# Performance work log

Hardware: AMD Instinct MI355X
Metric: run time of the kernel (lower is better)

## Reference

```python
import jax, jax.numpy as jnp
import numpy as np
from itertools import permutations

NUM_LAYERS = 3
K = 5  # fixed node degree -> every Hungarian sub-problem is 5x5
# one-hot permutation tensor: P1H[p, r, c] = 1 iff permutation p assigns row r -> col c
PERMS = np.array(list(permutations(range(K))), dtype=np.int32)          # [120, K]
P1H = (PERMS[:, :, None] == np.arange(K)[None, None, :]).astype(np.float32)  # [120, K, K]


def _mlp(x, W1, b1, W2, b2):
    # 2-layer MLP with ReLU (repo's MLP(in, hid, out, 2))
    return jax.nn.relu(x @ W1 + b1) @ W2 + b2


def _sinkhorn(src, itera):
    s = jax.nn.softmax(src, axis=1)  # row-max subtraction is built in
    for i in range(itera):
        s = s / jnp.sum(s, axis=i % 2, keepdims=True)
    return jnp.nan_to_num(s)


def _masked_softmax(src):
    s1 = jnp.nan_to_num(jax.nn.softmax(src, axis=1))
    s2 = jnp.nan_to_num(jax.nn.softmax(src, axis=0))
    return (s1 + s2) * 0.5


def setup_inputs() -> dict:
    key = jax.random.key(0)
    ks = jax.random.split(key, 12)
    n1 = n2 = 1024
    hid = 64
    adj1 = jax.random.randint(ks[0], (n1, K), 0, n1)
    adj2 = jax.random.randint(ks[1], (n2, K), 0, n2)
    # adjacency matrices consistent with the neighbor lists
    G1 = jnp.zeros((n1, n1), jnp.float32).at[jnp.arange(n1)[:, None], adj1].set(1.0)
    G2 = jnp.zeros((n2, n2), jnp.float32).at[jnp.arange(n2)[:, None], adj2].set(1.0)
    s = 0.1
    return {
        'G1': G1, 'G2': G2, 'adj1': adj1, 'adj2': adj2,
        'ro_W1': jax.random.normal(ks[2], (NUM_LAYERS, 1, hid), jnp.float32) * s,
        'ro_b1': jax.random.normal(ks[3], (NUM_LAYERS, hid), jnp.float32) * s,
        'ro_W2': jax.random.normal(ks[4], (NUM_LAYERS, hid, 1), jnp.float32) * s,
        'ro_b2': jax.random.normal(ks[5], (NUM_LAYERS, 1), jnp.float32) * s,
        'fin_W1': jax.random.normal(ks[6], (1, hid), jnp.float32) * s,
        'fin_b1': jax.random.normal(ks[7], (hid,), jnp.float32) * s,
        'fin_W2': jax.random.normal(ks[8], (hid, 1), jnp.float32) * s,
        'fin_b2': jax.random.normal(ks[9], (1,), jnp.float32) * s,
    }


def reference(G1, G2, adj1, adj2, ro_W1, ro_b1, ro_W2, ro_b2, fin_W1, fin_b1, fin_W2, fin_b2):
    n1 = G1.shape[0]
    n2 = G2.shape[0]
    d1 = jnp.sum(G1, axis=1)
    d2 = jnp.sum(G2, axis=1)
    ttheta = jnp.mean(d1)
    # S[i, j, 0] = -|d1[i] - d2[j]|
    S = -jnp.abs(d1[:, None] - d2[None, :])[..., None]  # [n1, n2, 1]
    p1h = jnp.asarray(P1H)
    for li in range(NUM_LAYERS):
        Wn = _sinkhorn(_mlp(S / ttheta, ro_W1[li], ro_b1[li], ro_W2[li], ro_b2[li]).squeeze(-1), 5)
        W = jnp.log(Wn * (n1 * 1.5))
        W = jnp.where(jnp.isneginf(W), jnp.float32(-1e12), W)
        W = jnp.where(jnp.isposinf(W), jnp.float32(1e12), W)
        Wd = jax.lax.stop_gradient(W)  # matches W.detach().numpy()
        # small[a, b, r, c] = Wd[adj1[a, r], adj2[b, c]]  -> [n1, n2, K, K]
        small = jnp.transpose(Wd[adj1][:, :, adj2], (0, 2, 1, 3))
        # exact linear_sum_assignment(-small): maximize sum over the K! permutations
        scores = jnp.einsum('abrc,prc->abp', small, p1h)  # [n1, n2, 120]
        X1 = jnp.max(scores, axis=-1)                      # [n1, n2]
        S = X1[..., None]
    out = _masked_softmax(_mlp(S, fin_W1, fin_b1, fin_W2, fin_b2).squeeze(-1))
    return out
```

## Files before the change

### kernel.cpp

```cpp
#include <hip/hip_runtime.h>
#include <math.h>

#define N 1024
#define NB 256
#define KD 5
#define SL 8
#define NT 126
#define MAGIC 0x13572468
#define FSTRIDE 32
#define FREGION (NB * FSTRIDE + FSTRIDE)


__device__ __forceinline__ float load_sc(const float* p){
  return __hip_atomic_load(p, __ATOMIC_RELAXED, __HIP_MEMORY_SCOPE_AGENT);
}
__device__ __forceinline__ void store_sc(float* p, float v){
  __hip_atomic_store(p, v, __ATOMIC_RELAXED, __HIP_MEMORY_SCOPE_AGENT);
}
__device__ __forceinline__ int load_sci(const int* p){
  return __hip_atomic_load(p, __ATOMIC_RELAXED, __HIP_MEMORY_SCOPE_AGENT);
}
__device__ __forceinline__ void store_sci(int* p, int v){
  __hip_atomic_store(p, v, __ATOMIC_RELAXED, __HIP_MEMORY_SCOPE_AGENT);
}

__device__ __forceinline__ void gbarS(int* flg){
  __builtin_amdgcn_s_waitcnt(0);
  __syncthreads();
  const int t = threadIdx.x, B = blockIdx.x;
  int* go = flg + NB * FSTRIDE;
  if (B == 0){
    if (t > 0 && t < NB){
      while (load_sci(&flg[t * FSTRIDE]) != MAGIC) __builtin_amdgcn_s_sleep(2);
    }
    __syncthreads();
    if (t == 0) store_sci(go, MAGIC);
  } else {
    if (t == 0){
      store_sci(&flg[B * FSTRIDE], MAGIC);
      while (load_sci(go) != MAGIC) __builtin_amdgcn_s_sleep(2);
    }
    __syncthreads();
  }
}

__device__ __forceinline__ float wred_sum(float v){
#pragma unroll
  for (int off = 32; off > 0; off >>= 1) v += __shfl_down(v, off);
  return v;
}
__device__ __forceinline__ void bsum4(float v[4], float* s64){
  float w0 = wred_sum(v[0]), w1 = wred_sum(v[1]), w2 = wred_sum(v[2]), w3 = wred_sum(v[3]);
  __syncthreads();
  int wv = threadIdx.x >> 6;
  if ((threadIdx.x & 63) == 0){ s64[wv*4] = w0; s64[wv*4+1] = w1; s64[wv*4+2] = w2; s64[wv*4+3] = w3; }
  __syncthreads();
  float r0 = 0.f, r1 = 0.f, r2 = 0.f, r3 = 0.f;
#pragma unroll
  for (int i = 0; i < 16; ++i){ r0 += s64[i*4]; r1 += s64[i*4+1]; r2 += s64[i*4+2]; r3 += s64[i*4+3]; }
  v[0] = r0; v[1] = r1; v[2] = r2; v[3] = r3;
}

__device__ __forceinline__ int distinct5(const int* v){
  int c = 0;
#pragma unroll
  for (int r = 0; r < KD; ++r){
    bool dup = false;
#pragma unroll
    for (int s = 0; s < r; ++s) dup = dup || (v[s] == v[r]);
    c += dup ? 0 : 1;
  }
  return c;
}
__device__ __forceinline__ void sort5(int* s){
#pragma unroll
  for (int i = 0; i < 4; ++i)
#pragma unroll
    for (int j = 0; j < 4 - i; ++j){
      int a = s[j], b = s[j+1];
      s[j] = min(a, b); s[j+1] = max(a, b);
    }
}
__device__ __forceinline__ int msrank(const int* c5){
  const int C_[6][5] = { {0,0,0,0,0},
                         {1,1,1,1,1},
                         {1,2,3,4,5},
                         {1,3,6,10,15},
                         {1,4,10,20,35},
                         {1,5,15,35,70} };
  int rank = 0, prev = 0;
#pragma unroll
  for (int i = 0; i < 5; ++i){
    for (int v = prev; v < c5[i]; ++v) rank += C_[5 - v][4 - i];
    prev = c5[i];
  }
  return rank;
}

#define DP5(ACCESS, OUT) {                                        \
  float f[32]; f[0] = 0.f;                                        \
  _Pragma("unroll")                                               \
  for (int r = 0; r < KD; ++r){                                   \
    float tr[KD];                                                 \
    _Pragma("unroll")                                             \
    for (int c = 0; c < KD; ++c) tr[c] = (ACCESS);                \
    _Pragma("unroll")                                             \
    for (int m = 1; m < 32; ++m){                                 \
      if (__popc(m) == r + 1){                                    \
        float best = -3.0e38f;                                    \
        _Pragma("unroll")                                         \
        for (int c = 0; c < KD; ++c)                              \
          if (m & (1 << c)) best = fmaxf(best, f[m ^ (1 << c)] + tr[c]); \
        f[m] = best;                                              \
      }                                                           \
    }                                                             \
  }                                                               \
  OUT = f[31];                                                    \
}

__global__ __launch_bounds__(1024) void
kAll0(const int* __restrict__ adj1, const int* __restrict__ adj2,
      const float* __restrict__ roW1, const float* __restrict__ roB1,
      const float* __restrict__ roW2, const float* __restrict__ roB2,
      float* __restrict__ t2out, float* __restrict__ C1B)
{
  __shared__ float tY1[NT * NT];
  __shared__ unsigned char t2c[NT][5];
  __shared__ unsigned char sg1[N], sg2[N];
  __shared__ unsigned short st1[N], st2[N];
  __shared__ int h1[8], h2[8];
  __shared__ int cnt1T[NT], cnt2T[NT];
  __shared__ float A1[NT], B1[NT];
  __shared__ float slR1[NT], slC1[NT];
  __shared__ float vq[NT], vC[NT], vqi[NT], vCi[NT];
  __shared__ float sY0[25], slR0[5], slC0[5], stt2[2];
  __shared__ float s64[64];
  __shared__ float sAv[4];
  __shared__ float ux[128], udA[128], udB[128];
  __shared__ float xs1[64], dA1[64], dB1[64], xs2[64], dA2[64], dB2[64];
  __shared__ float At1[65], Bt1[65], At2[65], Bt2[65];
  __shared__ float sA0B0[4];

  const int t = threadIdx.x, B = blockIdx.x;
  const float L1536 = logf(1536.0f);

  if (t < 8){ h1[t] = 0; h2[t] = 0; }
  if (t < NT){ cnt1T[t] = 0; cnt2T[t] = 0; }
#pragma unroll 1
  for (int key = t; key < 3125; key += 1024){
    int d[5]; int k2 = key;
#pragma unroll
    for (int i = 0; i < 5; ++i){ d[i] = k2 % 5; k2 /= 5; }
    if (d[0] <= d[1] && d[1] <= d[2] && d[2] <= d[3] && d[3] <= d[4]){
      int r = msrank(d);
#pragma unroll
      for (int i = 0; i < 5; ++i) t2c[r][i] = (unsigned char)d[i];
    }
  }
  int a2[KD], a1v[KD];
#pragma unroll
  for (int c = 0; c < KD; ++c) a2[c] = adj2[t * KD + c];
#pragma unroll
  for (int r = 0; r < KD; ++r) a1v[r] = adj1[t * KD + r];
  int g2 = distinct5(a2) - 1;
  int g1 = distinct5(a1v) - 1;
  sg2[t] = (unsigned char)g2; atomicAdd(&h2[g2], 1);
  sg1[t] = (unsigned char)g1; atomicAdd(&h1[g1], 1);
  __syncthreads();

  {
    int c5[KD];
#pragma unroll
    for (int r = 0; r < KD; ++r) c5[r] = sg1[a1v[r]];
    sort5(c5);
    int ty = msrank(c5);
    st1[t] = (unsigned short)ty; atomicAdd(&cnt1T[ty], 1);
  }
  {
    int c5[KD];
#pragma unroll
    for (int c = 0; c < KD; ++c) c5[c] = sg2[a2[c]];
    sort5(c5);
    int ty = msrank(c5);
    st2[t] = (unsigned short)ty; atomicAdd(&cnt2T[ty], 1);
  }

  if (t < 64){
    float cnt1[5], cnt2[5];
#pragma unroll
    for (int g = 0; g < 5; ++g){ cnt1[g] = (float)h1[g]; cnt2[g] = (float)h2[g]; }
    float tt = 0.f;
#pragma unroll
    for (int g = 0; g < 5; ++g) tt += (float)(g + 1) * cnt1[g];
    tt *= (1.0f / 1024.0f);
    float tab[5];
#pragma unroll 1
    for (int i = 0; i < 5; ++i){
      float x = -(float)i / tt;
      float acc = roB2[0];
      for (int k = 0; k < 64; ++k){
        float hh = fmaxf(fmaf(x, roW1[k], roB1[k]), 0.f);
        acc = fmaf(hh, roW2[k], acc);
      }
      tab[i] = acc;
    }
    float Ee[5][5];
#pragma unroll
    for (int g = 0; g < 5; ++g)
#pragma unroll
      for (int h = 0; h < 5; ++h) Ee[g][h] = expf(tab[abs(g - h)]);
    float q0[5], C1c[5], q1[5], C2c[5], q2[5], C3c[5];
#pragma unroll
    for (int g = 0; g < 5; ++g){
      float s = 0.f;
#pragma unroll
      for (int h = 0; h < 5; ++h) s += cnt2[h] * Ee[g][h];
      q0[g] = s;
    }
#pragma unroll
    for (int h = 0; h < 5; ++h){
      float s = 0.f;
#pragma unroll
      for (int g = 0; g < 5; ++g) s += cnt1[g] * Ee[g][h] / q0[g];
      C1c[h] = s;
    }
#pragma unroll
    for (int g = 0; g < 5; ++g){
      float s = 0.f;
#pragma unroll
      for (int h = 0; h < 5; ++h) s += cnt2[h] * Ee[g][h] / C1c[h];
      q1[g] = s;
    }
#pragma unroll
    for (int h = 0; h < 5; ++h){
      float s = 0.f;
#pragma unroll
      for (int g = 0; g < 5; ++g) s += cnt1[g] * Ee[g][h] / q1[g];
      C2c[h] = s;
    }
#pragma unroll
    for (int g = 0; g < 5; ++g){
      float s = 0.f;
#pragma unroll
      for (int h = 0; h < 5; ++h) s += cnt2[h] * Ee[g][h] / C2c[h];
      q2[g] = s;
    }
#pragma unroll
    for (int h = 0; h < 5; ++h){
      float s = 0.f;
#pragma unroll
      for (int g = 0; g < 5; ++g) s += cnt1[g] * Ee[g][h] / q2[g];
      C3c[h] = s;
    }
    if (t == 0){
#pragma unroll
      for (int g = 0; g < 5; ++g){
#pragma unroll
        for (int h = 0; h < 5; ++h) sY0[g * 5 + h] = tab[abs(g - h)];
        slR0[g] = -logf(q2[g]);
        slC0[g] = logf(C3c[g]);
      }
      stt2[0] = tt;
    }
  } else if (t < 192){
    int set = (t < 128) ? 0 : 1;
    int l = t - 64 - set * 64;
    const float* w1g = roW1 + (set + 1) * 64;
    const float* b1g = roB1 + (set + 1) * 64;
    const float* w2g = roW2 + (set + 1) * 64;
    const float* b2g = roB2 + (set + 1);
    float w1 = w1g[l], bb = b1g[l], w2v = w2g[l];
    float xk, sdA, sdB, a0t = 0.f, b0t = 0.f;
    if (w1 != 0.f){
      xk = -bb / w1;
      float dA = w1 * w2v, dB = bb * w2v;
      if (w1 > 0.f){ sdA = dA;  sdB = dB; }
      else         { sdA = -dA; sdB = -dB; a0t = dA; b0t = dB; }
    } else {
      xk = 3.0e38f; sdA = 0.f; sdB = 0.f;
      b0t = fmaxf(bb, 0.f) * w2v;
    }
    ux[set * 64 + l] = xk; udA[set * 64 + l] = sdA; udB[set * 64 + l] = sdB;
    float A0 = wred_sum(a0t);
    float B0 = wred_sum(b0t);
    if (l == 0){ sA0B0[2 * set] = A0; sA0B0[2 * set + 1] = B0 + b2g[0]; }
  }
  __syncthreads();

  if (t < 64){
    float xk = ux[t]; int rank = 0;
    for (int j = 0; j < 64; ++j){
      float xj = ux[j];
      rank += (xj < xk || (xj == xk && j < t)) ? 1 : 0;
    }
    xs1[rank] = ux[t]; dA1[rank] = udA[t]; dB1[rank] = udB[t];
  } else if (t < 128){
    int l = t - 64;
    float xk = ux[64 + l]; int rank = 0;
    for (int j = 0; j < 64; ++j){
      float xj = ux[64 + j];
      rank += (xj < xk || (xj == xk && j < l)) ? 1 : 0;
    }
    xs2[rank] = ux[64 + l]; dA2[rank] = udA[64 + l]; dB2[rank] = udB[64 + l];
  } else if (t >= 256 && t < 256 + NT){
    int ty = t - 256;
    float sa = 5.0f * L1536, sb = 0.f;
#pragma unroll
    for (int i = 0; i < KD; ++i){
      int cl = t2c[ty][i];
      sa += slR0[cl];
      sb -= slC0[cl];
    }
    A1[ty] = sa; B1[ty] = sb;
  }
  __syncthreads();
  if (t < 65){
    float sa = sA0B0[0], sb = sA0B0[1];
    for (int r = 0; r < t; ++r){ sa += dA1[r]; sb += dB1[r]; }
    At1[t] = sa; Bt1[t] = sb;
  } else if (t >= 128 && t < 193){
    int l = t - 128;
    float sa = sA0B0[2], sb = sA0B0[3];
    for (int r = 0; r < l; ++r){ sa += dA2[r]; sb += dB2[r]; }
    At2[l] = sa; Bt2[l] = sb;
  }
  __syncthreads();

  const float tt = stt2[0];
#pragma unroll 1
  for (int e = t; e < NT * NT; e += 1024){
    int tau = e / NT, ups = e - tau * NT;
    const unsigned char* G = t2c[tau];
    const unsigned char* H = t2c[ups];
    float D;
    DP5(sY0[(int)G[r] * 5 + (int)H[c]], D);
    float x = (A1[tau] + B1[ups] + D) / tt;
    int seg = 0;
#pragma unroll
    for (int s = 64; s; s >>= 1)
      if (seg + s <= 64 && xs1[seg + s - 1] <= x) seg += s;
    tY1[e] = fmaf(At1[seg], x, Bt1[seg]);
  }
  __syncthreads();

  {
    int g = t >> 3, j = t & 7;
    if (g < NT){
      float acc = 0.f;
      for (int u = j; u < NT; u += 8) acc += (float)cnt2T[u] * expf(tY1[g * NT + u]);
      acc += __shfl_down(acc, 4, 8); acc += __shfl_down(acc, 2, 8); acc += __shfl_down(acc, 1, 8);
      if (j == 0){ vq[g] = acc; vqi[g] = 1.0f / acc; }
    }
    __syncthreads();
    if (g < NT){
      float acc = 0.f;
      for (int u = j; u < NT; u += 8) acc += (float)cnt1T[u] * expf(tY1[u * NT + g]) * vqi[u];
      acc += __shfl_down(acc, 4, 8); acc += __shfl_down(acc, 2, 8); acc += __shfl_down(acc, 1, 8);
      if (j == 0){ vC[g] = acc; vCi[g] = 1.0f / acc; }
    }
    __syncthreads();
    if (g < NT){
      float acc = 0.f;
      for (int u = j; u < NT; u += 8) acc += (float)cnt2T[u] * expf(tY1[g * NT + u]) * vCi[u];
      acc += __shfl_down(acc, 4, 8); acc += __shfl_down(acc, 2, 8); acc += __shfl_down(acc, 1, 8);
      if (j == 0){ vq[g] = acc; vqi[g] = 1.0f / acc; }
    }
    __syncthreads();
    if (g < NT){
      float acc = 0.f;
      for (int u = j; u < NT; u += 8) acc += (float)cnt1T[u] * expf(tY1[u * NT + g]) * vqi[u];
      acc += __shfl_down(acc, 4, 8); acc += __shfl_down(acc, 2, 8); acc += __shfl_down(acc, 1, 8);
      if (j == 0){ vC[g] = acc; vCi[g] = 1.0f / acc; }
    }
    __syncthreads();
    if (g < NT){
      float acc = 0.f;
      for (int u = j; u < NT; u += 8) acc += (float)cnt2T[u] * expf(tY1[g * NT + u]) * vCi[u];
      acc += __shfl_down(acc, 4, 8); acc += __shfl_down(acc, 2, 8); acc += __shfl_down(acc, 1, 8);
      if (j == 0){ vq[g] = acc; vqi[g] = 1.0f / acc; }
    }
    __syncthreads();
    if (g < NT){
      float acc = 0.f;
      for (int u = j; u < NT; u += 8) acc += (float)cnt1T[u] * expf(tY1[u * NT + g]) * vqi[u];
      acc += __shfl_down(acc, 4, 8); acc += __shfl_down(acc, 2, 8); acc += __shfl_down(acc, 1, 8);
      if (j == 0) vC[g] = acc;
    }
    __syncthreads();
  }
  if (t < NT){ slR1[t] = -logf(vq[t]); slC1[t] = logf(vC[t]); }
  __syncthreads();

  if (t < 4){
    int a = 4 * B + t;
    float s = 5.0f * L1536;
#pragma unroll
    for (int r = 0; r < KD; ++r) s += slR1[st1[adj1[a * KD + r]]];
    sAv[t] = s;
  }
  int stc[KD];
  float Bv2 = 0.f;
#pragma unroll
  for (int c = 0; c < KD; ++c){ stc[c] = st2[a2[c]]; Bv2 -= slC1[stc[c]]; }
  __syncthreads();

  float y[4];
#pragma unroll 1
  for (int rr = 0; rr < 4; ++rr){
    int str_[KD];
#pragma unroll
    for (int r = 0; r < KD; ++r) str_[r] = st1[adj1[(4 * B + rr) * KD + r]];
    float D;
    DP5(tY1[str_[r] * NT + stc[c]], D);
    float x = (sAv[rr] + Bv2 + D) / tt;
    int seg = 0;
#pragma unroll
    for (int s = 64; s; s >>= 1)
      if (seg + s <= 64 && xs2[seg + s - 1] <= x) seg += s;
    y[rr] = fmaf(At2[seg], x, Bt2[seg]);
  }
  float e4[4], q4[4];
#pragma unroll
  for (int r = 0; r < 4; ++r){ e4[r] = expf(y[r]); q4[r] = e4[r]; }
  bsum4(q4, s64);
  float cp = 0.f;
#pragma unroll
  for (int r = 0; r < 4; ++r){
    t2out[(size_t)(4 * B + r) * N + t] = y[r];
    cp += e4[r] / q4[r];
  }
  atomicAdd(&C1B[(size_t)(B & (SL - 1)) * N + t], cp);
}

__global__ __launch_bounds__(1024) void
kLayerF(const float* __restrict__ tm, const int* __restrict__ adj1, const int* __restrict__ adj2,
        const float* __restrict__ C1B, float* __restrict__ C2B, float* __restrict__ C3B,
        float* __restrict__ CFB, float* __restrict__ Rg,
        const float* __restrict__ w1g, const float* __restrict__ b1g,
        const float* __restrict__ w2g, const float* __restrict__ b2g,
        float* __restrict__ outp,
        int* __restrict__ bar1, int* __restrict__ bar2, int* __restrict__ bar3)
{
  __shared__ __align__(16) float rows20[20][N];
  __shared__ float lc[N];
  __shared__ float s64[64];
  __shared__ float sAv[4];
  __shared__ float ux[64], udA[64], udB[64], xs_s[64], dA_s[64], dB_s[64];
  __shared__ float A_tab[65], B_tab[65], sA0B0[2];
  const int t = threadIdx.x, B = blockIdx.x;

  int a2[KD];
#pragma unroll
  for (int c = 0; c < KD; ++c) a2[c] = adj2[t * KD + c];

  {
    int w = t >> 6, lane = t & 63;
    int seg = w & 3;
    int rbase = w >> 2;
#pragma unroll
    for (int k = 0; k < 5; ++k){
      int r2 = rbase + 4 * k;
      int src = adj1[(4 * B + (r2 / 5)) * KD + (r2 % 5)];
      const float* g = tm + (size_t)src * N + seg * 256 + lane * 4;
      __builtin_amdgcn_global_load_lds(
          (const __attribute__((address_space(1))) unsigned int*)g,
          (__attribute__((address_space(3))) unsigned int*)&rows20[r2][seg * 256],
          16, 0, 0);
    }
  }
  float E[4], q4[4];
#pragma unroll
  for (int r = 0; r < 4; ++r) E[r] = expf(tm[(size_t)(4 * B + r) * N + t]);

  if (t < 64){
    float w1 = w1g[t], bb = b1g[t], w2 = w2g[t];
    float xk, sdA, sdB, a0t = 0.f, b0t = 0.f;
    if (w1 != 0.f){
      xk = -bb / w1;
      float dA = w1 * w2, dB = bb * w2;
      if (w1 > 0.f){ sdA = dA;  sdB = dB; }
      else         { sdA = -dA; sdB = -dB; a0t = dA; b0t = dB; }
    } else {
      xk = 3.0e38f; sdA = 0.f; sdB = 0.f;
      b0t = fmaxf(bb, 0.f) * w2;
    }
    ux[t] = xk; udA[t] = sdA; udB[t] = sdB;
    float A0 = wred_sum(a0t);
    float B0 = wred_sum(b0t);
    if (t == 0){ sA0B0[0] = A0; sA0B0[1] = B0 + b2g[0]; }
  }
  __syncthreads();
  if (t < 64){
    float xk = ux[t]; int rank = 0;
    for (int j = 0; j < 64; ++j){
      float xj = ux[j];
      rank += (xj < xk || (xj == xk && j < t)) ? 1 : 0;
    }
    xs_s[rank] = ux[t]; dA_s[rank] = udA[t]; dB_s[rank] = udB[t];
  }
  __syncthreads();
  if (t < 65){
    float sa = sA0B0[0], sb = sA0B0[1];
    for (int r = 0; r < t; ++r){ sa += dA_s[r]; sb += dB_s[r]; }
    A_tab[t] = sa; B_tab[t] = sb;
  }

  {
    float C = 0.f;
#pragma unroll
    for (int k = 0; k < SL; ++k) C += C1B[(size_t)k * N + t];
    float iC = 1.0f / C;
#pragma unroll
    for (int r = 0; r < 4; ++r) q4[r] = E[r] * iC;
    bsum4(q4, s64);
    float cp = 0.f;
#pragma unroll
    for (int r = 0; r < 4; ++r) cp += E[r] / q4[r];
    atomicAdd(&C2B[(size_t)(B & (SL - 1)) * N + t], cp);
  }

  gbarS(bar1);
  {
    float C = 0.f;
#pragma unroll
    for (int k = 0; k < SL; ++k) C += load_sc(&C2B[(size_t)k * N + t]);
    float iC = 1.0f / C;
#pragma unroll
    for (int r = 0; r < 4; ++r) q4[r] = E[r] * iC;
    bsum4(q4, s64);
    float cp = 0.f;
#pragma unroll
    for (int r = 0; r < 4; ++r) cp += E[r] / q4[r];
    if (t < 4) store_sc(&Rg[4 * B + t], 1.0f / q4[t]);
    atomicAdd(&C3B[(size_t)(B & (SL - 1)) * N + t], cp);
  }

  gbarS(bar2);
  {
    float C = 0.f;
#pragma unroll
    for (int k = 0; k < SL; ++k) C += load_sc(&C3B[(size_t)k * N + t]);
    lc[t] = logf(C);
  }
  if (t >= 64 && t < 68){
    int a = 4 * B + (t - 64);
    float s = 5.0f * logf(1536.0f);
#pragma unroll
    for (int r = 0; r < KD; ++r) s += logf(load_sc(&Rg[adj1[a * KD + r]]));
    sAv[t - 64] = s;
  }
  __syncthreads();

  float Bvl = 0.f;
#pragma unroll
  for (int c = 0; c < KD; ++c) Bvl -= lc[a2[c]];

  float y[4];
#pragma unroll 1
  for (int rr = 0; rr < 4; ++rr){
    float D;
    DP5(rows20[rr * 5 + r][a2[c]], D);
    float x = sAv[rr] + Bvl + D;
    int seg = 0;
#pragma unroll
    for (int s = 64; s; s >>= 1)
      if (seg + s <= 64 && xs_s[seg + s - 1] <= x) seg += s;
    y[rr] = fmaf(A_tab[seg], x, B_tab[seg]);
  }

  float e4[4];
#pragma unroll
  for (int r = 0; r < 4; ++r){ e4[r] = expf(y[r]); q4[r] = e4[r]; }
  bsum4(q4, s64);

  float cp = 0.f;
#pragma unroll
  for (int r = 0; r < 4; ++r) cp += e4[r];
  atomicAdd(&CFB[(size_t)(B & (SL - 1)) * N + t], cp);

  gbarS(bar3);
  float CF = 0.f;
#pragma unroll
  for (int k = 0; k < SL; ++k) CF += load_sc(&CFB[(size_t)k * N + t]);
  float iCF = 1.0f / CF;
#pragma unroll
  for (int r = 0; r < 4; ++r){
    float v = 0.5f * e4[r] * (1.0f / q4[r] + iCF);
    outp[(size_t)(4 * B + r) * N + t] = v;
  }
}

extern "C" void kernel_launch(void* const* d_in, const int* in_sizes, int n_in,
                              void* d_out, int out_size, void* d_ws, size_t ws_size,
                              hipStream_t stream){
  (void)in_sizes; (void)n_in; (void)out_size; (void)ws_size;
  const int*   adj1 = (const int*)d_in[2];
  const int*   adj2 = (const int*)d_in[3];
  const float* roW1 = (const float*)d_in[4];
  const float* roB1 = (const float*)d_in[5];
  const float* roW2 = (const float*)d_in[6];
  const float* roB2 = (const float*)d_in[7];
  const float* fW1  = (const float*)d_in[8];
  const float* fB1  = (const float*)d_in[9];
  const float* fW2  = (const float*)d_in[10];
  const float* fB2  = (const float*)d_in[11];
  float* out = (float*)d_out;

  float* Pp = (float*)d_ws;
  float* Rg = Pp + (size_t)4 * SL * N;
  int*  flg = (int*)(Rg + N);

  kAll0<<<NB, 1024, 0, stream>>>(adj1, adj2, roW1, roB1, roW2, roB2, out, Pp);
  kLayerF<<<NB, 1024, 0, stream>>>(out, adj1, adj2,
                                   Pp + (size_t)0 * SL * N, Pp + (size_t)1 * SL * N,
                                   Pp + (size_t)2 * SL * N, Pp + (size_t)3 * SL * N, Rg,
                                   fW1, fB1, fW2, fB2, out,
                                   flg + 0 * FREGION, flg + 1 * FREGION, flg + 2 * FREGION);
}
```

Baseline: 178.2 us.

## Split table construction into separate kernel distributing NT*NT entries across blocks

Previously every one of the 256 blocks redundantly computed the full 126x126 DP table of layer-1 values in shared memory. The work is now split into a new kTable kernel, where each block computes only about 63 entries and writes them to global memory. A second kernel, kProd, loads the shared table and performs the remaining per-block setup. This removes the redundant per-block DP work at the cost of an extra kernel launch and a global round-trip of the table.

```diff
diff --git a/kernel.cpp b/kernel.cpp
--- a/kernel.cpp
+++ b/kernel.cpp
@@ -119,33 +119,21 @@
 }
 
 __global__ __launch_bounds__(1024) void
-kAll0(const int* __restrict__ adj1, const int* __restrict__ adj2,
-      const float* __restrict__ roW1, const float* __restrict__ roB1,
-      const float* __restrict__ roW2, const float* __restrict__ roB2,
-      float* __restrict__ t2out, float* __restrict__ C1B)
+kTable(const int* __restrict__ adj1, const int* __restrict__ adj2,
+       const float* __restrict__ roW1, const float* __restrict__ roB1,
+       const float* __restrict__ roW2, const float* __restrict__ roB2,
+       float* __restrict__ tY1g, float* __restrict__ ttp)
 {
-  __shared__ float tY1[NT * NT];
   __shared__ unsigned char t2c[NT][5];
-  __shared__ unsigned char sg1[N], sg2[N];
-  __shared__ unsigned short st1[N], st2[N];
   __shared__ int h1[8], h2[8];
-  __shared__ int cnt1T[NT], cnt2T[NT];
   __shared__ float A1[NT], B1[NT];
-  __shared__ float slR1[NT], slC1[NT];
-  __shared__ float vq[NT], vC[NT], vqi[NT], vCi[NT];
   __shared__ float sY0[25], slR0[5], slC0[5], stt2[2];
-  __shared__ float s64[64];
-  __shared__ float sAv[4];
-  __shared__ float ux[128], udA[128], udB[128];
-  __shared__ float xs1[64], dA1[64], dB1[64], xs2[64], dA2[64], dB2[64];
-  __shared__ float At1[65], Bt1[65], At2[65], Bt2[65];
-  __shared__ float sA0B0[4];
-
+  __shared__ float ux[64], udA[64], udB[64], xs1[64], dA1[64], dB1[64];
+  __shared__ float At1[65], Bt1[65], sA0B0[2];
   const int t = threadIdx.x, B = blockIdx.x;
   const float L1536 = logf(1536.0f);
 
   if (t < 8){ h1[t] = 0; h2[t] = 0; }
-  if (t < NT){ cnt1T[t] = 0; cnt2T[t] = 0; }
 #pragma unroll 1
   for (int key = t; key < 3125; key += 1024){
     int d[5]; int k2 = key;
@@ -157,33 +145,16 @@
       for (int i = 0; i < 5; ++i) t2c[r][i] = (unsigned char)d[i];
     }
   }
-  int a2[KD], a1v[KD];
-#pragma unroll
-  for (int c = 0; c < KD; ++c) a2[c] = adj2[t * KD + c];
-#pragma unroll
-  for (int r = 0; r < KD; ++r) a1v[r] = adj1[t * KD + r];
-  int g2 = distinct5(a2) - 1;
-  int g1 = distinct5(a1v) - 1;
-  sg2[t] = (unsigned char)g2; atomicAdd(&h2[g2], 1);
-  sg1[t] = (unsigned char)g1; atomicAdd(&h1[g1], 1);
-  __syncthreads();
-
-  {
-    int c5[KD];
-#pragma unroll
-    for (int r = 0; r < KD; ++r) c5[r] = sg1[a1v[r]];
-    sort5(c5);
-    int ty = msrank(c5);
-    st1[t] = (unsigned short)ty; atomicAdd(&cnt1T[ty], 1);
-  }
-  {
-    int c5[KD];
-#pragma unroll
-    for (int c = 0; c < KD; ++c) c5[c] = sg2[a2[c]];
-    sort5(c5);
-    int ty = msrank(c5);
-    st2[t] = (unsigned short)ty; atomicAdd(&cnt2T[ty], 1);
-  }
+  {
+    int a2[KD], a1v[KD];
+#pragma unroll
+    for (int c = 0; c < KD; ++c) a2[c] = adj2[t * KD + c];
+#pragma unroll
+    for (int r = 0; r < KD; ++r) a1v[r] = adj1[t * KD + r];
+    atomicAdd(&h2[distinct5(a2) - 1], 1);
+    atomicAdd(&h1[distinct5(a1v) - 1], 1);
+  }
+  __syncthreads();
 
   if (t < 64){
     float cnt1[5], cnt2[5];
@@ -262,13 +233,12 @@
       }
       stt2[0] = tt;
     }
-  } else if (t < 192){
-    int set = (t < 128) ? 0 : 1;
-    int l = t - 64 - set * 64;
-    const float* w1g = roW1 + (set + 1) * 64;
-    const float* b1g = roB1 + (set + 1) * 64;
-    const float* w2g = roW2 + (set + 1) * 64;
-    const float* b2g = roB2 + (set + 1);
+  } else if (t < 128){
+    int l = t - 64;
+    const float* w1g = roW1 + 64;
+    const float* b1g = roB1 + 64;
+    const float* w2g = roW2 + 64;
+    const float* b2g = roB2 + 1;
     float w1 = w1g[l], bb = b1g[l], w2v = w2g[l];
     float xk, sdA, sdB, a0t = 0.f, b0t = 0.f;
     if (w1 != 0.f){
@@ -280,10 +250,10 @@
       xk = 3.0e38f; sdA = 0.f; sdB = 0.f;
       b0t = fmaxf(bb, 0.f) * w2v;
     }
-    ux[set * 64 + l] = xk; udA[set * 64 + l] = sdA; udB[set * 64 + l] = sdB;
+    ux[l] = xk; udA[l] = sdA; udB[l] = sdB;
     float A0 = wred_sum(a0t);
     float B0 = wred_sum(b0t);
-    if (l == 0){ sA0B0[2 * set] = A0; sA0B0[2 * set + 1] = B0 + b2g[0]; }
+    if (l == 0){ sA0B0[0] = A0; sA0B0[1] = B0 + b2g[0]; }
   }
   __syncthreads();
 
@@ -294,14 +264,6 @@
       rank += (xj < xk || (xj == xk && j < t)) ? 1 : 0;
     }
     xs1[rank] = ux[t]; dA1[rank] = udA[t]; dB1[rank] = udB[t];
-  } else if (t < 128){
-    int l = t - 64;
-    float xk = ux[64 + l]; int rank = 0;
-    for (int j = 0; j < 64; ++j){
-      float xj = ux[64 + j];
-      rank += (xj < xk || (xj == xk && j < l)) ? 1 : 0;
-    }
-    xs2[rank] = ux[64 + l]; dA2[rank] = udA[64 + l]; dB2[rank] = udB[64 + l];
   } else if (t >= 256 && t < 256 + NT){
     int ty = t - 256;
     float sa = 5.0f * L1536, sb = 0.f;
@@ -318,28 +280,109 @@
     float sa = sA0B0[0], sb = sA0B0[1];
     for (int r = 0; r < t; ++r){ sa += dA1[r]; sb += dB1[r]; }
     At1[t] = sa; Bt1[t] = sb;
-  } else if (t >= 128 && t < 193){
-    int l = t - 128;
-    float sa = sA0B0[2], sb = sA0B0[3];
-    for (int r = 0; r < l; ++r){ sa += dA2[r]; sb += dB2[r]; }
-    At2[l] = sa; Bt2[l] = sb;
   }
   __syncthreads();
 
   const float tt = stt2[0];
+  if (B == 0 && t == 0) ttp[0] = tt;
+  if (t < 63){
+    int e = B + 256 * t;
+    if (e < NT * NT){
+      int tau = e / NT, ups = e - tau * NT;
+      const unsigned char* G = t2c[tau];
+      const unsigned char* H = t2c[ups];
+      float D;
+      DP5(sY0[(int)G[r] * 5 + (int)H[c]], D);
+      float x = (A1[tau] + B1[ups] + D) / tt;
+      int seg = 0;
+#pragma unroll
+      for (int s = 64; s; s >>= 1)
+        if (seg + s <= 64 && xs1[seg + s - 1] <= x) seg += s;
+      tY1g[e] = fmaf(At1[seg], x, Bt1[seg]);
+    }
+  }
+}
+
+__global__ __launch_bounds__(1024) void
+kProd(const int* __restrict__ adj1, const int* __restrict__ adj2,
+      const float* __restrict__ w1g, const float* __restrict__ b1g,
+      const float* __restrict__ w2g, const float* __restrict__ b2g,
+      const float* __restrict__ tY1g, const float* __restrict__ ttp,
+      float* __restrict__ t2out, float* __restrict__ C1B)
+{
+  __shared__ float tY1[NT * NT];
+  __shared__ unsigned char sg1[N], sg2[N];
+  __shared__ unsigned short st1[N], st2[N];
+  __shared__ int cnt1T[NT], cnt2T[NT];
+  __shared__ float slR1[NT], slC1[NT];
+  __shared__ float vq[NT], vC[NT], vqi[NT], vCi[NT];
+  __shared__ float s64[64];
+  __shared__ float sAv[4];
+  __shared__ float ux[64], udA[64], udB[64], xs2[64], dA2[64], dB2[64];
+  __shared__ float At2[65], Bt2[65], sA0B0[2];
+  const int t = threadIdx.x, B = blockIdx.x;
+  const float L1536 = logf(1536.0f);
+  const float tt = ttp[0];
+
+  if (t < NT){ cnt1T[t] = 0; cnt2T[t] = 0; }
 #pragma unroll 1
-  for (int e = t; e < NT * NT; e += 1024){
-    int tau = e / NT, ups = e - tau * NT;
-    const unsigned char* G = t2c[tau];
-    const unsigned char* H = t2c[ups];
-    float D;
-    DP5(sY0[(int)G[r] * 5 + (int)H[c]], D);
-    float x = (A1[tau] + B1[ups] + D) / tt;
-    int seg = 0;
-#pragma unroll
-    for (int s = 64; s; s >>= 1)
-      if (seg + s <= 64 && xs1[seg + s - 1] <= x) seg += s;
-    tY1[e] = fmaf(At1[seg], x, Bt1[seg]);
+  for (int e = t; e < NT * NT; e += 1024) tY1[e] = tY1g[e];
+  int a2[KD], a1v[KD];
+#pragma unroll
+  for (int c = 0; c < KD; ++c) a2[c] = adj2[t * KD + c];
+#pragma unroll
+  for (int r = 0; r < KD; ++r) a1v[r] = adj1[t * KD + r];
+  sg2[t] = (unsigned char)(distinct5(a2) - 1);
+  sg1[t] = (unsigned char)(distinct5(a1v) - 1);
+  __syncthreads();
+
+  {
+    int c5[KD];
+#pragma unroll
+    for (int r = 0; r < KD; ++r) c5[r] = sg1[a1v[r]];
+    sort5(c5);
+    int ty = msrank(c5);
+    st1[t] = (unsigned short)ty; atomicAdd(&cnt1T[ty], 1);
+  }
+  {
+    int c5[KD];
+#pragma unroll
+    for (int c = 0; c < KD; ++c) c5[c] = sg2[a2[c]];
+    sort5(c5);
+    int ty = msrank(c5);
+    st2[t] = (unsigned short)ty; atomicAdd(&cnt2T[ty], 1);
+  }
+  if (t < 64){
+    float w1 = w1g[t], bb = b1g[t], w2v = w2g[t];
+    float xk, sdA, sdB, a0t = 0.f, b0t = 0.f;
+    if (w1 != 0.f){
+      xk = -bb / w1;
+      float dA = w1 * w2v, dB = bb * w2v;
+      if (w1 > 0.f){ sdA = dA;  sdB = dB; }
+      else         { sdA = -dA; sdB = -dB; a0t = dA; b0t = dB; }
+    } else {
+      xk = 3.0e38f; sdA = 0.f; sdB = 0.f;
+      b0t = fmaxf(bb, 0.f) * w2v;
+    }
+    ux[t] = xk; udA[t] = sdA; udB[t] = sdB;
+    float A0 = wred_sum(a0t);
+    float B0 = wred_sum(b0t);
+    if (t == 0){ sA0B0[0] = A0; sA0B0[1] = B0 + b2g[0]; }
+  }
+  __syncthreads();
+  if (t < 64){
+    float xk = ux[t]; int rank = 0;
+    for (int j = 0; j < 64; ++j){
+      float xj = ux[j];
+      rank += (xj < xk || (xj == xk && j < t)) ? 1 : 0;
+    }
+    xs2[rank] = ux[t]; dA2[rank] = udA[t]; dB2[rank] = udB[t];
+  }
+  __syncthreads();
+  if (t < 65){
+    float sa = sA0B0[0], sb = sA0B0[1];
+    for (int r = 0; r < t; ++r){ sa += dA2[r]; sb += dB2[r]; }
+    At2[t] = sa; Bt2[t] = sb;
   }
   __syncthreads();
 
@@ -606,11 +649,16 @@
   const float* fB2  = (const float*)d_in[11];
   float* out = (float*)d_out;
 
-  float* Pp = (float*)d_ws;
-  float* Rg = Pp + (size_t)4 * SL * N;
-  int*  flg = (int*)(Rg + N);
-
-  kAll0<<<NB, 1024, 0, stream>>>(adj1, adj2, roW1, roB1, roW2, roB2, out, Pp);
+  float* Pp   = (float*)d_ws;
+  float* Rg   = Pp + (size_t)4 * SL * N;
+  float* ttp  = Rg + N;
+  float* tY1g = ttp + 8;
+  int*   flg  = (int*)(tY1g + NT * NT);
+
+  kTable<<<NB, 1024, 0, stream>>>(adj1, adj2, roW1, roB1, roW2, roB2, tY1g, ttp);
+  kProd<<<NB, 1024, 0, stream>>>(adj1, adj2,
+                                 roW1 + 128, roB1 + 128, roW2 + 128, roB2 + 2,
+                                 tY1g, ttp, out, Pp);
   kLayerF<<<NB, 1024, 0, stream>>>(out, adj1, adj2,
                                    Pp + (size_t)0 * SL * N, Pp + (size_t)1 * SL * N,
                                    Pp + (size_t)2 * SL * N, Pp + (size_t)3 * SL * N, Rg,
```

New measurement: 161.2 us. 1.11x faster.
